# Performance work log

Measured on AMD Instinct MI355X. Metric: run time of the kernel, lower is better.

The kernel has to match this reference:

```python
import jax, jax.numpy as jnp
import numpy as np

BATCH, SEQ, EMBED = 8, 1024, 2048
HEADS, LATENT = 16, 512
HEAD_DIM = EMBED // HEADS            # 128
NOPE = HEAD_DIM // 4                 # 32 (qk_rope_dim=96 is even, no adjust)
ROPE_D = HEAD_DIM - NOPE             # 96
THETA = 10000.0


def _rope_tables(seq_len):
    # matches torch: freqs over arange(0, rope_dim, 2)/rope_dim
    freqs = 1.0 / THETA ** (jnp.arange(0, ROPE_D, 2, dtype=jnp.float32) / ROPE_D)
    emb = jnp.arange(seq_len, dtype=jnp.float32)[:, None] * freqs[None, :]  # [S, ROPE_D//2]
    return jnp.cos(emb), jnp.sin(emb)


def _apply_rope(x, cos, sin):
    # x: [B,H,S,D]; cos/sin: [S,D//2]. NOTE: original concatenates halves (non-interleaved output).
    xe, xo = x[..., ::2], x[..., 1::2]
    return jnp.concatenate([xe * cos - xo * sin, xo * cos + xe * sin], axis=-1)


def setup_inputs() -> dict:
    key = jax.random.key(0)
    ks = jax.random.split(key, 5)
    x = jax.random.normal(ks[0], (BATCH, SEQ, EMBED), jnp.float32)
    Wq = jax.random.normal(ks[1], (EMBED, EMBED), jnp.float32) * 0.02
    Wkv_down = jax.random.normal(ks[2], (EMBED, LATENT), jnp.float32) * 0.02
    Wk_up = jax.random.normal(ks[3], (LATENT, EMBED), jnp.float32) * 0.02
    Wv_up = jax.random.normal(ks[4], (LATENT, EMBED), jnp.float32) * 0.02
    return {"x": x, "Wq": Wq, "Wkv_down": Wkv_down, "Wk_up": Wk_up, "Wv_up": Wv_up}


def reference(x, Wq, Wkv_down, Wk_up, Wv_up):
    B, S, E = x.shape
    # projections (weights stored [in, out], equivalent to nn.Linear math)
    q = (x @ Wq).reshape(B, S, HEADS, HEAD_DIM).transpose(0, 2, 1, 3)   # [B,H,S,D]
    q_nope, q_rope = q[..., :NOPE], q[..., NOPE:]
    c_kv = x @ Wkv_down                                                  # [B,S,latent]
    k = (c_kv @ Wk_up).reshape(B, S, HEADS, HEAD_DIM).transpose(0, 2, 1, 3)
    v = (c_kv @ Wv_up).reshape(B, S, HEADS, HEAD_DIM).transpose(0, 2, 1, 3)
    k_nope, k_rope = k[..., :NOPE], k[..., NOPE:]

    cos, sin = _rope_tables(S)
    q_rope = _apply_rope(q_rope, cos, sin)
    k_rope = _apply_rope(k_rope, cos, sin)

    qf = jnp.concatenate([q_nope, q_rope], axis=-1)
    kf = jnp.concatenate([k_nope, k_rope], axis=-1)

    scale = jnp.float32(1.0 / np.sqrt(HEAD_DIM))
    scores = jnp.einsum('bhqd,bhkd->bhqk', qf, kf) * scale
    causal = jnp.triu(jnp.ones((S, S), dtype=bool), k=1)  # past_length=0
    scores = jnp.where(causal, -jnp.inf, scores)
    weights = jax.nn.softmax(scores, axis=-1)
    out = jnp.einsum('bhqk,bhkd->bhqd', weights, v)
    return out.transpose(0, 2, 1, 3).reshape(B, S, E)
```

## Files before the change

kernel.cpp:

```cpp
#include <hip/hip_runtime.h>
#include <stdint.h>

typedef unsigned short u16;
typedef __bf16 bf16x8 __attribute__((ext_vector_type(8)));
typedef float    f32x4 __attribute__((ext_vector_type(4)));
typedef unsigned short u16x8 __attribute__((ext_vector_type(8)));
typedef unsigned short u16x4 __attribute__((ext_vector_type(4)));

#define BB 8
#define SS 1024
#define EE 2048
#define HH 16
#define DD 128

__device__ __forceinline__ u16 f2bf(float f){
  union { float f; unsigned u; } v; v.f = f;
  unsigned r = v.u + 0x7FFFu + ((v.u >> 16) & 1u);
  return (u16)(r >> 16);
}
__device__ __forceinline__ float bf2f(u16 h){
  union { unsigned u; float f; } v; v.u = ((unsigned)h) << 16;
  return v.f;
}
__device__ __forceinline__ bf16x8 ld8(const u16* p){
  return __builtin_bit_cast(bf16x8, *(const u16x8*)p);
}

typedef __attribute__((address_space(1))) const unsigned int gas_u32;
typedef __attribute__((address_space(3))) unsigned int las_u32;
__device__ __forceinline__ void g2l16(const u16* g, u16* l){
  __builtin_amdgcn_global_load_lds((gas_u32*)g, (las_u32*)l, 16, 0, 0);
}

#define BARRIER() asm volatile("s_barrier" ::: "memory")
#define VMC(n)    asm volatile("s_waitcnt vmcnt(" #n ")" ::: "memory")

__device__ __forceinline__ void trB(const float* __restrict__ W, u16* __restrict__ Wt,
                                    int K, int N, int bx, int by,
                                    float (*t)[33], int tid){
  int c = tid & 31, r = tid >> 5;
  #pragma unroll
  for (int i = 0; i < 32; i += 8)
    t[r+i][c] = W[(size_t)(by*32 + r + i)*N + bx*32 + c];
  __syncthreads();
  #pragma unroll
  for (int i = 0; i < 32; i += 8)
    Wt[(size_t)(bx*32 + r + i)*K + by*32 + c] = f2bf(t[c][r+i]);
}

__global__ __launch_bounds__(256) void prep(const float* __restrict__ x, u16* __restrict__ xb,
    const float* __restrict__ Wq,   u16* __restrict__ WqT,
    const float* __restrict__ Wkvd, u16* __restrict__ WkvdT,
    const float* __restrict__ Wku,  u16* __restrict__ WkuT,
    const float* __restrict__ Wvu,  u16* __restrict__ WvuT,
    float* __restrict__ cosb, float* __restrict__ sinb){
  __shared__ float t[32][33];
  const int bid = blockIdx.x, tid = threadIdx.x;
  if (bid < 8192){
    int i = (bid*256 + tid)*8;
    float4 v0 = *(const float4*)(x + i);
    float4 v1 = *(const float4*)(x + i + 4);
    u16x8 o;
    o[0]=f2bf(v0.x); o[1]=f2bf(v0.y); o[2]=f2bf(v0.z); o[3]=f2bf(v0.w);
    o[4]=f2bf(v1.x); o[5]=f2bf(v1.y); o[6]=f2bf(v1.z); o[7]=f2bf(v1.w);
    *(u16x8*)(xb + i) = o;
  } else if (bid < 12288){
    int k = bid - 8192;  trB(Wq,   WqT,   EE,  EE,  k & 63, k >> 6, t, tid);
  } else if (bid < 13312){
    int k = bid - 12288; trB(Wkvd, WkvdT, EE,  512, k & 15, k >> 4, t, tid);
  } else if (bid < 14336){
    int k = bid - 13312; trB(Wku,  WkuT,  512, EE,  k & 63, k >> 6, t, tid);
  } else if (bid < 15360){
    int k = bid - 14336; trB(Wvu,  WvuT,  512, EE,  k & 63, k >> 6, t, tid);
  } else {
    int i = (bid - 15360)*256 + tid;
    if (i < SS*48){
      int s = i / 48, j = i % 48;
      float freq = powf(10000.0f, -((float)(2*j)) / 96.0f);
      float e = (float)s * freq;
      cosb[i] = cosf(e);
      sinb[i] = sinf(e);
    }
  }
}

__global__ __launch_bounds__(256) void rope_apply2(u16* __restrict__ qp,
                                                   u16* __restrict__ kp,
                                                   const float* __restrict__ cosb,
                                                   const float* __restrict__ sinb){
  u16* base = blockIdx.y ? kp : qp;
  int t = blockIdx.x*256 + threadIdx.x;
  int row = t >> 4, h = t & 15, s = row & (SS-1);
  u16* p = base + (size_t)row*EE + h*DD + 32;
  float e[48], o[48];
  #pragma unroll
  for (int c = 0; c < 12; c++){
    u16x8 v = *(const u16x8*)(p + c*8);
    #pragma unroll
    for (int j = 0; j < 4; j++){
      e[c*4 + j] = bf2f(v[2*j]);
      o[c*4 + j] = bf2f(v[2*j+1]);
    }
  }
  u16 ob[96];
  #pragma unroll
  for (int j = 0; j < 48; j++){
    float cs = cosb[s*48 + j], sn = sinb[s*48 + j];
    ob[j]      = f2bf(e[j]*cs - o[j]*sn);
    ob[48 + j] = f2bf(o[j]*cs + e[j]*sn);
  }
  #pragma unroll
  for (int c = 0; c < 12; c++)
    *(u16x8*)(p + c*8) = *(const u16x8*)(ob + c*8);
}

__global__ __launch_bounds__(256) void gemm_bt(const u16* __restrict__ A,
    const u16* __restrict__ Bt, u16* __restrict__ C, int M, int N, int K){
  __shared__ u16 Al[128*32];
  __shared__ u16 Bl[128*32];
  const int tid = threadIdx.x;
  const int lane = tid & 63, w = tid >> 6;
  const int wr = w >> 1, wc = w & 1;
  const int l15 = lane & 15, l4 = lane >> 4;
  const int id = blockIdx.y * 4 + blockIdx.x;
  const int xcd = id & 7, j = id >> 3;
  const int bm = (xcd*8 + (j >> 2)) * 128;
  const int bn = (j & 3) * 128;
  const int srow = tid >> 2;
  const int skc  = (tid & 3) * 8;
  const u16* ga = A  + (size_t)(bm + srow)*K + skc;
  const u16* gb = Bt + (size_t)(bn + srow)*K + skc;
  u16* la = Al + w*512;
  u16* lb = Bl + w*512;
  f32x4 acc[4][4] = {};
  for (int k0 = 0; k0 < K; k0 += 32){
    __syncthreads();
    g2l16(ga + k0,          la);
    g2l16(ga + 64*K + k0,   la + 2048);
    g2l16(gb + k0,          lb);
    g2l16(gb + 64*K + k0,   lb + 2048);
    __syncthreads();
    bf16x8 af[4], bfr[4];
    #pragma unroll
    for (int m = 0; m < 4; m++) af[m]  = ld8(Al + (wr*64 + m*16 + l15)*32 + l4*8);
    #pragma unroll
    for (int n = 0; n < 4; n++) bfr[n] = ld8(Bl + (wc*64 + n*16 + l15)*32 + l4*8);
    #pragma unroll
    for (int m = 0; m < 4; m++)
      #pragma unroll
      for (int n = 0; n < 4; n++)
        acc[m][n] = __builtin_amdgcn_mfma_f32_16x16x32_bf16(af[m], bfr[n], acc[m][n], 0, 0, 0);
  }
  #pragma unroll
  for (int m = 0; m < 4; m++)
    #pragma unroll
    for (int n = 0; n < 4; n++)
      #pragma unroll
      for (int r = 0; r < 4; r++){
        int row = bm + wr*64 + m*16 + l4*4 + r;
        int col = bn + wc*64 + n*16 + l15;
        C[(size_t)row*N + col] = f2bf(acc[m][n][r]);
      }
}

#define AFR(ab, mf, ks) ld8(&AL[ab][wr][((mf)*16 + l15)*64 + ((((ks)*4 + l4) ^ r7) << 3)])
#define BFR(bb, nf, ks) ld8(&BL[bb][wc>>1][(((wc&1)*64 + (nf)*16 + l15))*64 + ((((ks)*4 + l4) ^ r7) << 3)])

#define STAGE_A(ab, h, kt) stage2(aRow, (h), (kt), K, &AL[ab][h][0], wj0)
#define STAGE_A2(ab, kt)   do{ STAGE_A(ab, 0, kt); STAGE_A(ab, 1, kt); }while(0)
#define STAGE_B(bb, h, kt) stage2(bRow, (h), (kt), K, &BL[bb][h][0], wj0)

__device__ __forceinline__ void stage2(const u16* rowbase, int h, int kt, int K,
                                       u16* lds, int wj0){
  const u16* g = rowbase + (size_t)h*128*K + kt*64;
  g2l16(g,               lds + wj0*512);
  g2l16(g + (size_t)8*K, lds + wj0*512 + 512);
}

#define PHASE(ab, q, LOADB, STAGE, DOVM) do{                                       \
  bf16x8 a00 = AFR(ab, 2*(q)  , 0);                                               \
  bf16x8 a01 = AFR(ab, 2*(q)  , 1);                                               \
  bf16x8 a10 = AFR(ab, 2*(q)+1, 0);                                               \
  bf16x8 a11 = AFR(ab, 2*(q)+1, 1);                                               \
  if (LOADB){                                                                      \
    _Pragma("unroll")                                                              \
    for (int nf = 0; nf < 4; nf++){ bq[nf][0]=BFR(ab,nf,0); bq[nf][1]=BFR(ab,nf,1); } \
  }                                                                                \
  STAGE;                                                                           \
  if (DOVM) VMC(4);                                                                \
  BARRIER();                                                                       \
  __builtin_amdgcn_s_setprio(1);                                                   \
  _Pragma("unroll")                                                                \
  for (int nf = 0; nf < 4; nf++){                                                  \
    acc[2*(q)][nf]   = __builtin_amdgcn_mfma_f32_16x16x32_bf16(a00, bq[nf][0], acc[2*(q)][nf],0,0,0);   \
    acc[2*(q)+1][nf] = __builtin_amdgcn_mfma_f32_16x16x32_bf16(a10, bq[nf][0], acc[2*(q)+1][nf],0,0,0); \
  }                                                                                \
  _Pragma("unroll")                                                                \
  for (int nf = 0; nf < 4; nf++){                                                  \
    acc[2*(q)][nf]   = __builtin_amdgcn_mfma_f32_16x16x32_bf16(a01, bq[nf][1], acc[2*(q)][nf],0,0,0);   \
    acc[2*(q)+1][nf] = __builtin_amdgcn_mfma_f32_16x16x32_bf16(a11, bq[nf][1], acc[2*(q)+1][nf],0,0,0); \
  }                                                                                \
  __builtin_amdgcn_s_setprio(0);                                                   \
  BARRIER();                                                                       \
  __builtin_amdgcn_sched_barrier(0);                                               \
}while(0)

template<int NLOOP>
__global__ __launch_bounds__(512, 2) void gemm8(const u16* __restrict__ A,
    const u16* __restrict__ Bt, u16* __restrict__ C0, u16* __restrict__ C1,
    int K, int Nout0, int Nout1, int nsplit, int vt){
  __shared__ u16 AL[2][2][128*64];
  __shared__ u16 BL[2][2][128*64];
  const int tid = threadIdx.x, lane = tid & 63, w = tid >> 6;
  const int wr = w >> 2, wc = w & 3;
  const int l15 = lane & 15, l4 = lane >> 4;
  const int r7 = l15 & 7;
  const int nbx = gridDim.x;
  const int id  = blockIdx.y * nbx + blockIdx.x;
  const int xcd = id & 7, j = id >> 3;
  const int rpx = gridDim.y >> 3;
  const int bn0 = (j % nbx) * 256;
  const int bm  = (xcd*rpx + (j / nbx)) * 256;
  const int wj0 = w*2;
  const int cswz = (lane & 7) ^ (lane >> 3);
  const u16* aRow = A + (size_t)(bm + wj0*8 + (lane>>3))*K + cswz*8;

  const int nkt = K >> 6;
  const int niter = nkt >> 1;

  #pragma unroll
  for (int t2 = 0; t2 < NLOOP; t2++){
    const int bn = bn0 + t2 * nbx * 256;
    const u16* bRow = Bt + (size_t)(bn + wj0*8 + (lane>>3))*K + cswz*8;

    STAGE_A2(0, 0);
    STAGE_B(0, 0, 0); STAGE_B(0, 1, 0);
    STAGE_B(1, 0, 1); STAGE_B(1, 1, 1);
    VMC(4);
    BARRIER();

    f32x4 acc[8][4] = {};
    bf16x8 bq[4][2];

    for (int it = 0; it < niter; ++it){
      const int kt1 = 2*it + 1;
      int kt2 = 2*it + 2; if (kt2 >= nkt) kt2 -= nkt;
      int kt3 = 2*it + 3; if (kt3 >= nkt) kt3 -= nkt;
      PHASE(0, 0, 1, STAGE_A2(1, kt1),    0);
      PHASE(0, 1, 0, STAGE_B(0, 0, kt2),  0);
      PHASE(0, 2, 0, STAGE_B(0, 1, kt2),  0);
      PHASE(0, 3, 0, ;,                   1);
      PHASE(1, 0, 1, STAGE_A2(0, kt2),    0);
      PHASE(1, 1, 0, STAGE_B(1, 0, kt3),  0);
      PHASE(1, 2, 0, STAGE_B(1, 1, kt3),  0);
      PHASE(1, 3, 0, ;,                   1);
    }
    asm volatile("s_waitcnt vmcnt(0)" ::: "memory");

    if (vt && bn >= nsplit){
      const int bcol = bn - nsplit;
      #pragma unroll
      for (int mf = 0; mf < 8; mf++)
        #pragma unroll
        for (int nf = 0; nf < 4; nf++){
          int row0 = bm + wr*128 + mf*16 + l4*4;
          int col  = bcol + wc*64 + nf*16 + l15;
          int bh = (row0 >> 10)*16 + (col >> 7);
          int d  = col & 127;
          int s  = row0 & 1023;
          u16x4 pk;
          #pragma unroll
          for (int r = 0; r < 4; r++) pk[r] = f2bf(acc[mf][nf][r]);
          *(u16x4*)(C1 + (((size_t)(bh*128 + d)) << 10) + s) = pk;
        }
    } else {
      u16* Cd = (bn < nsplit) ? C0 : C1;
      const int No = (bn < nsplit) ? Nout0 : Nout1;
      const int bcol = (bn < nsplit) ? bn : bn - nsplit;
      #pragma unroll
      for (int mf = 0; mf < 8; mf++)
        #pragma unroll
        for (int nf = 0; nf < 4; nf++)
          #pragma unroll
          for (int r = 0; r < 4; r++){
            int row = bm + wr*128 + mf*16 + l4*4 + r;
            int col = bcol + wc*64 + nf*16 + l15;
            Cd[(size_t)row*No + col] = f2bf(acc[mf][nf][r]);
          }
    }
  }
}

#define PLW 40

__global__ __launch_bounds__(512) void attn(const u16* __restrict__ qp,
                                            const u16* __restrict__ kp,
                                            const u16* __restrict__ vpT,
                                            float* __restrict__ out){
  __shared__ u16 Kl[2][64*128];
  __shared__ u16 Vl[2][128*64];
  __shared__ u16 Pl[8][16*PLW];
  const int tid = threadIdx.x, lane = tid & 63, w = tid >> 6;
  const int l15 = lane & 15, l4 = lane >> 4;
  const int qt = 7 - blockIdx.y;
  const int bh = blockIdx.x;
  const int b = bh >> 4, h = bh & 15;
  const int qbase = qt*128;
  const int qmin = qbase + w*16;
  const int qg = qmin + l15;
  const float c = 0.12751920700948998f;
  const float THR = 62.7f;

  const size_t rowq = (size_t)(b*SS + qg)*EE + h*DD;
  bf16x8 qf[4];
  #pragma unroll
  for (int kk = 0; kk < 4; kk++) qf[kk] = ld8(qp + rowq + kk*32 + l4*8);
  #pragma unroll
  for (int kk = 0; kk < 4; kk++) asm volatile("" : "+v"(qf[kk]));

  f32x4 ao[8] = {};
  float mi = -3e38f, li = 0.0f;

  const int ntiles = 2*qt + 2;
  const int vcc = lane & 7;

  #pragma unroll
  for (int q = 0; q < 2; q++){
    int r = w*8 + q*4 + (lane>>4);
    g2l16(kp + (size_t)(b*SS + r)*EE + h*DD + (((lane&15) ^ (r&7))<<3),
          &Kl[0][0] + w*1024 + q*512);
    int d = w*16 + q*8 + (lane>>3);
    g2l16(vpT + (size_t)(bh*DD + d)*SS + ((vcc ^ (d&7))<<3),
          &Vl[0][0] + w*1024 + q*512);
  }

  for (int t = 0; t < ntiles; t++){
    const int kv0 = t*64;
    const int buf = t & 1;
    {
      const int kvn = (t + 1 < ntiles) ? kv0 + 64 : kv0;
      #pragma unroll
      for (int q = 0; q < 2; q++){
        int r = w*8 + q*4 + (lane>>4);
        g2l16(kp + (size_t)(b*SS + kvn + r)*EE + h*DD + (((lane&15) ^ (r&7))<<3),
              &Kl[buf^1][0] + w*1024 + q*512);
        int d = w*16 + q*8 + (lane>>3);
        g2l16(vpT + (size_t)(bh*DD + d)*SS + kvn + ((vcc ^ (d&7))<<3),
              &Vl[buf^1][0] + w*1024 + q*512);
      }
    }
    VMC(4);
    BARRIER();

    if (kv0 <= qmin + 15){
      float sv[4][4];
      __builtin_amdgcn_s_setprio(1);
      #pragma unroll
      for (int nt = 0; nt < 4; nt++){
        f32x4 sacc = {};
        #pragma unroll
        for (int kk = 0; kk < 4; kk++){
          bf16x8 kf = ld8(&Kl[buf][0] + (nt*16 + l15)*128 + (((kk*4 + l4) ^ (l15&7))<<3));
          sacc = __builtin_amdgcn_mfma_f32_16x16x32_bf16(kf, qf[kk], sacc, 0, 0, 0);
        }
        #pragma unroll
        for (int r = 0; r < 4; r++) sv[nt][r] = sacc[r];
      }
      __builtin_amdgcn_s_setprio(0);
      if (kv0 + 63 > qmin){
        #pragma unroll
        for (int nt = 0; nt < 4; nt++)
          #pragma unroll
          for (int r = 0; r < 4; r++){
            int kg = kv0 + nt*16 + l4*4 + r;
            if (kg > qg) sv[nt][r] = -3e38f;
          }
      }
      float mx = sv[0][0];
      #pragma unroll
      for (int nt = 0; nt < 4; nt++)
        #pragma unroll
        for (int r = 0; r < 4; r++) mx = fmaxf(mx, sv[nt][r]);
      mx = fmaxf(mx, __shfl_xor(mx, 16));
      mx = fmaxf(mx, __shfl_xor(mx, 32));
      if (__any(mx > mi + THR)){
        float mnew = fmaxf(mi, mx);
        float alpha = __builtin_amdgcn_exp2f((mi - mnew)*c);
        li *= alpha;
        #pragma unroll
        for (int n8 = 0; n8 < 8; n8++) ao[n8] *= alpha;
        mi = mnew;
      }
      const float mnc = mi*c;
      float pout[4][4];
      float rs = 0.0f;
      #pragma unroll
      for (int nt = 0; nt < 4; nt++)
        #pragma unroll
        for (int r = 0; r < 4; r++){
          float pv = __builtin_amdgcn_exp2f(__builtin_fmaf(sv[nt][r], c, -mnc));
          pout[nt][r] = pv; rs += pv;
        }
      rs += __shfl_xor(rs, 16);
      rs += __shfl_xor(rs, 32);
      li += rs;
      #pragma unroll
      for (int kk = 0; kk < 2; kk++){
        #pragma unroll
        for (int ntl = 0; ntl < 2; ntl++){
          int nt = kk*2 + ntl;
          u16x4 pk;
          #pragma unroll
          for (int r = 0; r < 4; r++) pk[r] = f2bf(pout[nt][r]);
          *(u16x4*)(&Pl[w][l15*PLW + ntl*16 + l4*4]) = pk;
        }
        bf16x8 pa = ld8(&Pl[w][l15*PLW + l4*8]);
        __builtin_amdgcn_s_setprio(1);
        #pragma unroll
        for (int n8 = 0; n8 < 8; n8++){
          bf16x8 vf = ld8(&Vl[buf][0] + (n8*16 + l15)*64 + (((kk*4 + l4) ^ (l15&7))<<3));
          ao[n8] = __builtin_amdgcn_mfma_f32_16x16x32_bf16(vf, pa, ao[n8], 0, 0, 0);
        }
        __builtin_amdgcn_s_setprio(0);
      }
    }
    BARRIER();
  }
  asm volatile("s_waitcnt vmcnt(0)" ::: "memory");

  const float inv = 1.0f / li;
  const size_t orow = (size_t)(b*SS + qg)*EE + h*DD;
  #pragma unroll
  for (int n8 = 0; n8 < 8; n8++){
    f32x4 o = ao[n8]*inv;
    *(float4*)(out + orow + n8*16 + l4*4) = __builtin_bit_cast(float4, o);
  }
}

extern "C" void kernel_launch(void* const* d_in, const int* in_sizes, int n_in,
                              void* d_out, int out_size, void* d_ws, size_t ws_size,
                              hipStream_t stream){
  const float* x    = (const float*)d_in[0];
  const float* Wq   = (const float*)d_in[1];
  const float* Wkvd = (const float*)d_in[2];
  const float* Wku  = (const float*)d_in[3];
  const float* Wvu  = (const float*)d_in[4];
  float* out = (float*)d_out;
  char* ws = (char*)d_ws;

  u16*   xb    = (u16*)  (ws);
  u16*   WqT   = (u16*)  (ws +  33554432);
  u16*   WkvdT = (u16*)  (ws +  41943040);
  u16*   WkuT  = (u16*)  (ws +  44040192);
  u16*   WvuT  = (u16*)  (ws +  46137344);
  float* cosb  = (float*)(ws +  48234496);
  float* sinb  = (float*)(ws +  48431104);
  u16*   qp    = (u16*)  (ws +  48627712);
  u16*   ckv   = (u16*)  (ws +  82182144);
  u16*   kp    = (u16*)  (ws +  90570752);
  u16*   vpT   = (u16*)  (ws + 124125184);

  prep<<<15552, 256, 0, stream>>>(x, xb, Wq, WqT, Wkvd, WkvdT,
                                  Wku, WkuT, Wvu, WvuT, cosb, sinb);

  gemm8<1><<<dim3(EE/256, (BB*SS)/256), 512, 0, stream>>>(xb, WqT, qp, qp,
                                                          EE, EE, EE, EE, 0);
  gemm_bt<<<dim3(512/128, (BB*SS)/128), 256, 0, stream>>>(xb, WkvdT, ckv, BB*SS, 512, EE);
  gemm8<2><<<dim3(2048/256, (BB*SS)/256), 512, 0, stream>>>(ckv, WkuT, kp, vpT,
                                                            512, EE, 0, EE, 1);

  rope_apply2<<<dim3((BB*SS*HH)/256, 2), 256, 0, stream>>>(qp, kp, cosb, sinb);

  attn<<<dim3(BB*HH, SS/128), 512, 0, stream>>>(qp, kp, vpT, out);
}
```

Measured before the change: 283.8 us.

## Process two 16-row query fragments per wave in attention, halving waves per block

The attention kernel now runs 4 waves per block instead of 8, and each wave handles 32 query rows as two 16-row MFMA fragments. Each K and V fragment read from LDS is reused for two MFMAs, cutting LDS read traffic per FLOP. Each wave now issues twice as many global-to-LDS loads, and the added accumulators raise register pressure. Fewer waves per block may also reduce latency hiding, and causal skipping becomes coarser because it is decided per 32 rows.

```diff
diff --git a/kernel.cpp b/kernel.cpp
--- a/kernel.cpp
+++ b/kernel.cpp
@@ -293,45 +293,51 @@
 
 #define PLW 40
 
-__global__ __launch_bounds__(512) void attn(const u16* __restrict__ qp,
+__global__ __launch_bounds__(256) void attn(const u16* __restrict__ qp,
                                             const u16* __restrict__ kp,
                                             const u16* __restrict__ vpT,
                                             float* __restrict__ out){
   __shared__ u16 Kl[2][64*128];
   __shared__ u16 Vl[2][128*64];
-  __shared__ u16 Pl[8][16*PLW];
+  __shared__ u16 Pl[4][32*PLW];
   const int tid = threadIdx.x, lane = tid & 63, w = tid >> 6;
   const int l15 = lane & 15, l4 = lane >> 4;
   const int qt = 7 - blockIdx.y;
   const int bh = blockIdx.x;
   const int b = bh >> 4, h = bh & 15;
   const int qbase = qt*128;
-  const int qmin = qbase + w*16;
-  const int qg = qmin + l15;
+  const int qmin = qbase + w*32;
   const float c = 0.12751920700948998f;
   const float THR = 62.7f;
 
-  const size_t rowq = (size_t)(b*SS + qg)*EE + h*DD;
-  bf16x8 qf[4];
-  #pragma unroll
-  for (int kk = 0; kk < 4; kk++) qf[kk] = ld8(qp + rowq + kk*32 + l4*8);
-  #pragma unroll
-  for (int kk = 0; kk < 4; kk++) asm volatile("" : "+v"(qf[kk]));
-
-  f32x4 ao[8] = {};
-  float mi = -3e38f, li = 0.0f;
+  bf16x8 qf[2][4];
+  #pragma unroll
+  for (int f = 0; f < 2; f++){
+    const size_t rowq = (size_t)(b*SS + qmin + f*16 + l15)*EE + h*DD;
+    #pragma unroll
+    for (int kk = 0; kk < 4; kk++) qf[f][kk] = ld8(qp + rowq + kk*32 + l4*8);
+  }
+  #pragma unroll
+  for (int f = 0; f < 2; f++)
+    #pragma unroll
+    for (int kk = 0; kk < 4; kk++) asm volatile("" : "+v"(qf[f][kk]));
+
+  f32x4 ao[2][8] = {};
+  float mi[2] = {-3e38f, -3e38f}, li[2] = {0.0f, 0.0f};
 
   const int ntiles = 2*qt + 2;
-  const int vcc = lane & 7;
-
-  #pragma unroll
-  for (int q = 0; q < 2; q++){
-    int r = w*8 + q*4 + (lane>>4);
+
+  #pragma unroll
+  for (int q = 0; q < 4; q++){
+    int r = w*16 + q*4 + (lane>>4);
     g2l16(kp + (size_t)(b*SS + r)*EE + h*DD + (((lane&15) ^ (r&7))<<3),
-          &Kl[0][0] + w*1024 + q*512);
-    int d = w*16 + q*8 + (lane>>3);
-    g2l16(vpT + (size_t)(bh*DD + d)*SS + ((vcc ^ (d&7))<<3),
-          &Vl[0][0] + w*1024 + q*512);
+          &Kl[0][0] + w*2048 + q*512);
+  }
+  #pragma unroll
+  for (int q = 0; q < 4; q++){
+    int d = w*32 + q*8 + (lane>>3);
+    g2l16(vpT + (size_t)(bh*DD + d)*SS + (((lane&7) ^ (d&7))<<3),
+          &Vl[0][0] + w*2048 + q*512);
   }
 
   for (int t = 0; t < ntiles; t++){
@@ -340,86 +346,110 @@
     {
       const int kvn = (t + 1 < ntiles) ? kv0 + 64 : kv0;
       #pragma unroll
-      for (int q = 0; q < 2; q++){
-        int r = w*8 + q*4 + (lane>>4);
+      for (int q = 0; q < 4; q++){
+        int r = w*16 + q*4 + (lane>>4);
         g2l16(kp + (size_t)(b*SS + kvn + r)*EE + h*DD + (((lane&15) ^ (r&7))<<3),
-              &Kl[buf^1][0] + w*1024 + q*512);
-        int d = w*16 + q*8 + (lane>>3);
-        g2l16(vpT + (size_t)(bh*DD + d)*SS + kvn + ((vcc ^ (d&7))<<3),
-              &Vl[buf^1][0] + w*1024 + q*512);
-      }
-    }
-    VMC(4);
+              &Kl[buf^1][0] + w*2048 + q*512);
+      }
+      #pragma unroll
+      for (int q = 0; q < 4; q++){
+        int d = w*32 + q*8 + (lane>>3);
+        g2l16(vpT + (size_t)(bh*DD + d)*SS + kvn + (((lane&7) ^ (d&7))<<3),
+              &Vl[buf^1][0] + w*2048 + q*512);
+      }
+    }
+    VMC(8);
     BARRIER();
 
-    if (kv0 <= qmin + 15){
-      float sv[4][4];
+    if (kv0 <= qmin + 31){
+      float sv[2][4][4];
       __builtin_amdgcn_s_setprio(1);
       #pragma unroll
       for (int nt = 0; nt < 4; nt++){
-        f32x4 sacc = {};
+        f32x4 s0 = {}, s1 = {};
         #pragma unroll
         for (int kk = 0; kk < 4; kk++){
           bf16x8 kf = ld8(&Kl[buf][0] + (nt*16 + l15)*128 + (((kk*4 + l4) ^ (l15&7))<<3));
-          sacc = __builtin_amdgcn_mfma_f32_16x16x32_bf16(kf, qf[kk], sacc, 0, 0, 0);
+          s0 = __builtin_amdgcn_mfma_f32_16x16x32_bf16(kf, qf[0][kk], s0, 0, 0, 0);
+          s1 = __builtin_amdgcn_mfma_f32_16x16x32_bf16(kf, qf[1][kk], s1, 0, 0, 0);
         }
         #pragma unroll
-        for (int r = 0; r < 4; r++) sv[nt][r] = sacc[r];
+        for (int r = 0; r < 4; r++){ sv[0][nt][r] = s0[r]; sv[1][nt][r] = s1[r]; }
       }
       __builtin_amdgcn_s_setprio(0);
       if (kv0 + 63 > qmin){
         #pragma unroll
+        for (int f = 0; f < 2; f++){
+          int qgf = qmin + f*16 + l15;
+          #pragma unroll
+          for (int nt = 0; nt < 4; nt++)
+            #pragma unroll
+            for (int r = 0; r < 4; r++){
+              int kg = kv0 + nt*16 + l4*4 + r;
+              if (kg > qgf) sv[f][nt][r] = -3e38f;
+            }
+        }
+      }
+      float mx[2];
+      int need = 0;
+      #pragma unroll
+      for (int f = 0; f < 2; f++){
+        float m0 = sv[f][0][0];
+        #pragma unroll
         for (int nt = 0; nt < 4; nt++)
           #pragma unroll
+          for (int r = 0; r < 4; r++) m0 = fmaxf(m0, sv[f][nt][r]);
+        m0 = fmaxf(m0, __shfl_xor(m0, 16));
+        m0 = fmaxf(m0, __shfl_xor(m0, 32));
+        mx[f] = m0;
+        need |= (m0 > mi[f] + THR);
+      }
+      if (__any(need)){
+        #pragma unroll
+        for (int f = 0; f < 2; f++){
+          float mnew = fmaxf(mi[f], mx[f]);
+          float alpha = __builtin_amdgcn_exp2f((mi[f] - mnew)*c);
+          li[f] *= alpha;
+          #pragma unroll
+          for (int n8 = 0; n8 < 8; n8++) ao[f][n8] *= alpha;
+          mi[f] = mnew;
+        }
+      }
+      #pragma unroll
+      for (int f = 0; f < 2; f++){
+        const float mnc = mi[f]*c;
+        float rs = 0.0f;
+        #pragma unroll
+        for (int nt = 0; nt < 4; nt++)
+          #pragma unroll
           for (int r = 0; r < 4; r++){
-            int kg = kv0 + nt*16 + l4*4 + r;
-            if (kg > qg) sv[nt][r] = -3e38f;
+            float pv = __builtin_amdgcn_exp2f(__builtin_fmaf(sv[f][nt][r], c, -mnc));
+            sv[f][nt][r] = pv; rs += pv;
           }
-      }
-      float mx = sv[0][0];
-      #pragma unroll
-      for (int nt = 0; nt < 4; nt++)
-        #pragma unroll
-        for (int r = 0; r < 4; r++) mx = fmaxf(mx, sv[nt][r]);
-      mx = fmaxf(mx, __shfl_xor(mx, 16));
-      mx = fmaxf(mx, __shfl_xor(mx, 32));
-      if (__any(mx > mi + THR)){
-        float mnew = fmaxf(mi, mx);
-        float alpha = __builtin_amdgcn_exp2f((mi - mnew)*c);
-        li *= alpha;
-        #pragma unroll
-        for (int n8 = 0; n8 < 8; n8++) ao[n8] *= alpha;
-        mi = mnew;
-      }
-      const float mnc = mi*c;
-      float pout[4][4];
-      float rs = 0.0f;
-      #pragma unroll
-      for (int nt = 0; nt < 4; nt++)
-        #pragma unroll
-        for (int r = 0; r < 4; r++){
-          float pv = __builtin_amdgcn_exp2f(__builtin_fmaf(sv[nt][r], c, -mnc));
-          pout[nt][r] = pv; rs += pv;
-        }
-      rs += __shfl_xor(rs, 16);
-      rs += __shfl_xor(rs, 32);
-      li += rs;
+        rs += __shfl_xor(rs, 16);
+        rs += __shfl_xor(rs, 32);
+        li[f] += rs;
+      }
       #pragma unroll
       for (int kk = 0; kk < 2; kk++){
         #pragma unroll
-        for (int ntl = 0; ntl < 2; ntl++){
-          int nt = kk*2 + ntl;
-          u16x4 pk;
-          #pragma unroll
-          for (int r = 0; r < 4; r++) pk[r] = f2bf(pout[nt][r]);
-          *(u16x4*)(&Pl[w][l15*PLW + ntl*16 + l4*4]) = pk;
-        }
-        bf16x8 pa = ld8(&Pl[w][l15*PLW + l4*8]);
+        for (int f = 0; f < 2; f++)
+          #pragma unroll
+          for (int ntl = 0; ntl < 2; ntl++){
+            int nt = kk*2 + ntl;
+            u16x4 pk;
+            #pragma unroll
+            for (int r = 0; r < 4; r++) pk[r] = f2bf(sv[f][nt][r]);
+            *(u16x4*)(&Pl[w][(f*16 + l15)*PLW + ntl*16 + l4*4]) = pk;
+          }
+        bf16x8 pa0 = ld8(&Pl[w][l15*PLW + l4*8]);
+        bf16x8 pa1 = ld8(&Pl[w][(16 + l15)*PLW + l4*8]);
         __builtin_amdgcn_s_setprio(1);
         #pragma unroll
         for (int n8 = 0; n8 < 8; n8++){
           bf16x8 vf = ld8(&Vl[buf][0] + (n8*16 + l15)*64 + (((kk*4 + l4) ^ (l15&7))<<3));
-          ao[n8] = __builtin_amdgcn_mfma_f32_16x16x32_bf16(vf, pa, ao[n8], 0, 0, 0);
+          ao[0][n8] = __builtin_amdgcn_mfma_f32_16x16x32_bf16(vf, pa0, ao[0][n8], 0, 0, 0);
+          ao[1][n8] = __builtin_amdgcn_mfma_f32_16x16x32_bf16(vf, pa1, ao[1][n8], 0, 0, 0);
         }
         __builtin_amdgcn_s_setprio(0);
       }
@@ -428,12 +458,15 @@
   }
   asm volatile("s_waitcnt vmcnt(0)" ::: "memory");
 
-  const float inv = 1.0f / li;
-  const size_t orow = (size_t)(b*SS + qg)*EE + h*DD;
-  #pragma unroll
-  for (int n8 = 0; n8 < 8; n8++){
-    f32x4 o = ao[n8]*inv;
-    *(float4*)(out + orow + n8*16 + l4*4) = __builtin_bit_cast(float4, o);
+  #pragma unroll
+  for (int f = 0; f < 2; f++){
+    const float inv = 1.0f / li[f];
+    const size_t orow = (size_t)(b*SS + qmin + f*16 + l15)*EE + h*DD;
+    #pragma unroll
+    for (int n8 = 0; n8 < 8; n8++){
+      f32x4 o = ao[f][n8]*inv;
+      *(float4*)(out + orow + n8*16 + l4*4) = __builtin_bit_cast(float4, o);
+    }
   }
 }
 
@@ -471,5 +504,5 @@
 
   rope_apply2<<<dim3((BB*SS*HH)/256, 2), 256, 0, stream>>>(qp, kp, cosb, sinb);
 
-  attn<<<dim3(BB*HH, SS/128), 512, 0, stream>>>(qp, kp, vpT, out);
-}
+  attn<<<dim3(BB*HH, SS/128), 256, 0, stream>>>(qp, kp, vpT, out);
+}
```

New measurement: 314.5 us. 1.11x slower.
